# Performance work log

Measured on AMD Instinct MI355X. Metric: run time of the kernel, lower is better.

## Reference

```python
import jax, jax.numpy as jnp
import numpy as np

T_STEPS = 4096
N_CLASSES = 8192
TGT_LEN = 512
BLANK = 0
NEG = jnp.float32(-1e30)  # finite 'log zero' so grads stay nan-free


def setup_inputs() -> dict:
    key = jax.random.key(0)
    k1, k2 = jax.random.split(key)
    logits = jax.random.normal(k1, (T_STEPS, 1, N_CLASSES), dtype=jnp.float32)
    targets = jax.random.randint(k2, (TGT_LEN,), 0, N_CLASSES, dtype=jnp.int32)
    return {
        "logits": logits,
        "targets": targets,
        "input_lengths": T_STEPS,
        "target_lengths": TGT_LEN,
    }


def reference(logits, targets, input_lengths, target_lengths):
    # logits: [T, 1, C] -> log_probs [T, C]
    lp = jax.nn.log_softmax(logits, axis=2)[:, 0, :]
    L = target_lengths                      # static Python int
    tgt = targets[:L]
    S = 2 * L + 1
    # interleave blanks: [blank, y1, blank, y2, ..., blank]
    tw = jnp.full((S,), BLANK, dtype=tgt.dtype).at[1::2].set(tgt)

    # skip transition (s-2 -> s) allowed iff tw[s] != blank and tw[s] != tw[s-2]
    tw_m2 = jnp.concatenate([jnp.full((2,), -1, tw.dtype), tw[:-2]])
    allow_skip = (tw != BLANK) & (tw != tw_m2)

    # emission log-probs per state: [T, S]
    emit = lp[:, tw]

    alpha0 = jnp.full((S,), NEG).at[0].set(lp[0, BLANK])
    if S > 1:
        alpha0 = alpha0.at[1].set(lp[0, tw[1]])

    pad1 = jnp.full((1,), NEG)
    pad2 = jnp.full((2,), NEG)

    def step(a_prev, e_t):
        s1 = jnp.concatenate([pad1, a_prev[:-1]])
        s2 = jnp.concatenate([pad2, a_prev[:-2]])
        s2 = jnp.where(allow_skip, s2, NEG)
        a = jax.nn.logsumexp(jnp.stack([a_prev, s1, s2]), axis=0) + e_t
        return a, a

    _, alphas = jax.lax.scan(step, alpha0, emit[1:])
    alpha = jnp.concatenate([alpha0[None, :], alphas], axis=0)  # [T, S]

    final = jax.nn.logsumexp(alpha[input_lengths - 1, -2:])
    return -final
```

## Files before the change

### kernel.cpp

```cpp
#include <hip/hip_runtime.h>
#include <hip/hip_bf16.h>


#define T_STEPS 4096
#define N_CLASSES 8192
#define ROWB 2048
#define DG 12
#define DEPTH 16
#define INV_LN2 1.4426950408889634f
#define LN2F 0.6931471805599453f

static __device__ __forceinline__ float wredMax(float v) {
#pragma unroll
  for (int d = 32; d >= 1; d >>= 1) v = fmaxf(v, __shfl_xor(v, d, 64));
  return v;
}
static __device__ __forceinline__ float wredSum(float v) {
#pragma unroll
  for (int d = 32; d >= 1; d >>= 1) v += __shfl_xor(v, d, 64);
  return v;
}

#define FEXP2(x) __builtin_amdgcn_exp2f(x)
#define FLOG2(x) __builtin_amdgcn_logf(x)

__global__ __launch_bounds__(256) void ctc_emit(const float* __restrict__ logits,
                                                const int* __restrict__ targets,
                                                unsigned int* __restrict__ P,
                                                float* __restrict__ cvec) {
  __shared__ __align__(16) float row[N_CLASSES];
  __shared__ float red[4];
  const int t = blockIdx.x;
  const int tid = threadIdx.x;
  const int lane = tid & 63, wid = tid >> 6;
  const float4* src = (const float4*)(logits + (size_t)t * N_CLASSES);

  float4 v[8];
  float lmax = -3.0e38f;
#pragma unroll
  for (int k = 0; k < 8; ++k) {
    v[k] = src[tid + 256 * k];
    ((float4*)row)[tid + 256 * k] = v[k];
    lmax = fmaxf(lmax, fmaxf(fmaxf(v[k].x, v[k].y), fmaxf(v[k].z, v[k].w)));
  }
  lmax = wredMax(lmax);
  if (lane == 0) red[wid] = lmax;
  __syncthreads();
  const float rowmax = fmaxf(fmaxf(red[0], red[1]), fmaxf(red[2], red[3]));
  const float m2 = rowmax * INV_LN2;

  float acc = 0.f;
#pragma unroll
  for (int k = 0; k < 8; ++k) {
    acc += FEXP2(fmaf(v[k].x, INV_LN2, -m2));
    acc += FEXP2(fmaf(v[k].y, INV_LN2, -m2));
    acc += FEXP2(fmaf(v[k].z, INV_LN2, -m2));
    acc += FEXP2(fmaf(v[k].w, INV_LN2, -m2));
  }
  acc = wredSum(acc);
  __syncthreads();
  if (lane == 0) red[wid] = acc;
  __syncthreads();
  const float Z = red[0] + red[1] + red[2] + red[3];
  const float denom2 = m2 + FLOG2(Z);

  const float eb2 = fmaf(row[0], INV_LN2, -denom2);
  float et2[2];
  float gmax = eb2;
#pragma unroll
  for (int j = 0; j < 2; ++j) {
    const int p = tid + 256 * j;
    et2[j] = fmaf(row[targets[p]], INV_LN2, -denom2);
    gmax = fmaxf(gmax, et2[j]);
  }
  gmax = wredMax(gmax);
  __syncthreads();
  if (lane == 0) red[wid] = gmax;
  __syncthreads();
  const float ct = fmaxf(fmaxf(red[0], red[1]), fmaxf(red[2], red[3]));

  __hip_bfloat162* Prow = (__hip_bfloat162*)(P + (size_t)t * (ROWB / 4));
  __hip_bfloat162 pr;
  pr.x = __float2bfloat16(FEXP2(eb2 - ct));
#pragma unroll
  for (int j = 0; j < 2; ++j) {
    const int p = tid + 256 * j;
    pr.y = __float2bfloat16(FEXP2(et2[j] - ct));
    Prow[(p >> 3) | ((p & 7) << 6)] = pr;
  }
  if (tid == 0) cvec[t] = ct;
}

#define UNPK_LO(u) __uint_as_float((u) << 16)
#define UNPK_HI(u) __uint_as_float((u) & 0xFFFF0000u)

template <int DIRN>
static __device__ __forceinline__ void scan_half(const unsigned char* __restrict__ Pb,
                                                 const int* __restrict__ targets,
                                                 unsigned char* lbuf,
                                                 float* __restrict__ rawOut,
                                                 int* __restrict__ omOut) {
  const int lane = threadIdx.x;

  float al[8];
#pragma unroll
  for (int k = 0; k < 8; ++k) {
    const int kg = 8 * lane + k;
    if (DIRN == 0) {
      const int c = targets[kg];
      const int cm1 = (kg == 0) ? -1 : targets[kg - 1];
      al[k] = (c != 0 && c != cm1) ? 1.0f : 0.0f;
    } else {
      if (kg == 0) {
        al[k] = 0.0f;
      } else {
        const int c = targets[512 - kg];
        const int cm1 = targets[511 - kg];
        al[k] = (c != 0 && c != cm1) ? 1.0f : 0.0f;
      }
    }
  }

  float a[16], b[16], a16 = 0.f, b16;
#pragma unroll
  for (int j = 0; j < 16; ++j) a[j] = 0.f;
  if (lane == 0) {
    const unsigned int pv0 = *(const unsigned int*)(
        Pb + (DIRN ? ((size_t)(T_STEPS - 1) * ROWB + 4 * 511) : (size_t)0));
    a[0] = __uint_as_float((pv0 & 0xFFFFu) << 16);
    a[1] = __uint_as_float(pv0 & 0xFFFF0000u);
  }
  int omega = 0;
  int wprev = 0;
  int wd = 0;
  float Lraw = __shfl_up(a[15], 1, 64);

  const long long gstep = DIRN ? -(long long)ROWB : (long long)ROWB;
  const unsigned char* gp =
      Pb + (DIRN ? (size_t)(T_STEPS - 2) * ROWB : (size_t)ROWB) + 16 * lane;

#define STAGE_ROW(slot)                                                        \
  {                                                                            \
    unsigned char* lq = lbuf + (size_t)(slot) * ROWB;                          \
    __builtin_amdgcn_global_load_lds(                                          \
        (const __attribute__((address_space(1))) void*)gp,                     \
        (__attribute__((address_space(3))) void*)lq, 16, 0, 0);                \
    __builtin_amdgcn_global_load_lds(                                          \
        (const __attribute__((address_space(1))) void*)(gp + 1024),            \
        (__attribute__((address_space(3))) void*)(lq + 1024), 16, 0, 0);       \
    gp += gstep;                                                               \
  }

  const int rl = DIRN ? (63 - lane) : lane;

#define LOADSLOT(slot, R0, R1, R2, R3, R4, R5, R6, R7)                         \
  {                                                                            \
    const __attribute__((address_space(3))) unsigned int* sp =                 \
        (const __attribute__((address_space(3))) unsigned int*)(               \
            lbuf + (size_t)(slot) * ROWB);                                     \
    R0 = sp[rl + (DIRN ? 448 : 0)];                                            \
    R1 = sp[rl + (DIRN ? 384 : 64)];                                           \
    R2 = sp[rl + (DIRN ? 320 : 128)];                                          \
    R3 = sp[rl + (DIRN ? 256 : 192)];                                          \
    R4 = sp[rl + (DIRN ? 192 : 256)];                                          \
    R5 = sp[rl + (DIRN ? 128 : 320)];                                          \
    R6 = sp[rl + (DIRN ? 64 : 384)];                                           \
    R7 = sp[rl + (DIRN ? 0 : 448)];                                            \
  }

#pragma unroll
  for (int tt = 1; tt <= DG; ++tt) STAGE_ROW(tt & 15);

  unsigned int p0, p1, p2, p3, p4, p5, p6, p7;
  unsigned int q0, q1, q2, q3, q4, q5, q6, q7;
  asm volatile("s_waitcnt vmcnt(16)" ::: "memory");
  LOADSLOT(1, p0, p1, p2, p3, p4, p5, p6, p7);
  LOADSLOT(2, q0, q1, q2, q3, q4, q5, q6, q7);

  int t = 1;

#define STEP_HEAD(R0, R1, R2, R3, R4, R5, R6, R7)                              \
    const unsigned int x0 = R0, x1 = R1, x2 = R2, x3 = R3, x4 = R4, x5 = R5,   \
                       x6 = R6, x7 = R7;                                       \
    STAGE_ROW((t + DG) & 15);                                                  \
    asm volatile("s_waitcnt vmcnt(16)" ::: "memory");                          \
    LOADSLOT((t + 2) & 15, R0, R1, R2, R3, R4, R5, R6, R7);

#define BODY_MID(A, B)                                                         \
    B[2] = (A[2] + A[1]) * UNPK_LO(x1);                                        \
    B[3] = fmaf(al[1], A[1], A[3] + A[2]) * UNPK_HI(x1);                       \
    B[4] = (A[4] + A[3]) * UNPK_LO(x2);                                        \
    B[5] = fmaf(al[2], A[3], A[5] + A[4]) * UNPK_HI(x2);                       \
    B[6] = (A[6] + A[5]) * UNPK_LO(x3);                                        \
    B[7] = fmaf(al[3], A[5], A[7] + A[6]) * UNPK_HI(x3);                       \
    B[8] = (A[8] + A[7]) * UNPK_LO(x4);                                        \
    B[9] = fmaf(al[4], A[7], A[9] + A[8]) * UNPK_HI(x4);                       \
    B[10] = (A[10] + A[9]) * UNPK_LO(x5);                                      \
    B[11] = fmaf(al[5], A[9], A[11] + A[10]) * UNPK_HI(x5);                    \
    B[12] = (A[12] + A[11]) * UNPK_LO(x6);                                     \
    B[13] = fmaf(al[6], A[11], A[13] + A[12]) * UNPK_HI(x6);                   \
    B[14] = (A[14] + A[13]) * UNPK_LO(x7);

#define STEPF(A, A16, B, B16, R0, R1, R2, R3, R4, R5, R6, R7)                  \
  {                                                                            \
    STEP_HEAD(R0, R1, R2, R3, R4, R5, R6, R7)                                  \
    B[15] = fmaf(al[7], A[13], A[15] + A[14]) * UNPK_HI(x7);                   \
    B16 = (lane == 63) ? (A16 + A[15]) * UNPK_LO(x7) : 0.f;                    \
    float newL = __shfl_up(B[15], 1, 64);                                      \
    float La = (lane == 0) ? 0.f : ldexpf(Lraw, wd);                           \
    B[0] = (A[0] + La) * UNPK_LO(x0);                                          \
    B[1] = fmaf(al[0], La, A[1] + A[0]) * UNPK_HI(x0);                         \
    BODY_MID(A, B)                                                             \
    Lraw = newL;                                                               \
    ++t;                                                                       \
  }

#define STEPS(A, A16, B, B16, R0, R1, R2, R3, R4, R5, R6, R7)                  \
  {                                                                            \
    STEP_HEAD(R0, R1, R2, R3, R4, R5, R6, R7)                                  \
    float La = (lane == 0) ? 0.f : ldexpf(Lraw, wd);                           \
    B[15] = fmaf(al[7], A[13], A[15] + A[14]) * UNPK_HI(x7);                   \
    B16 = (lane == 63) ? (A16 + A[15]) * UNPK_LO(x7) : 0.f;                    \
    B[0] = (A[0] + La) * UNPK_LO(x0);                                          \
    B[1] = fmaf(al[0], La, A[1] + A[0]) * UNPK_HI(x0);                         \
    BODY_MID(A, B)                                                             \
    float m = 0.f;                                                             \
    _Pragma("unroll") for (int j = 0; j < 16; ++j) m = fmaxf(m, B[j]);         \
    if (lane == 63) m = fmaxf(m, B16);                                         \
    if (m > 0.f) {                                                             \
      const int e = (int)((__float_as_uint(m) >> 23) & 255u);                  \
      const int shift = 127 - e;                                               \
      _Pragma("unroll") for (int j = 0; j < 16; ++j) B[j] = ldexpf(B[j], shift); \
      B16 = ldexpf(B16, shift);                                                \
      omega += shift;                                                          \
    } else {                                                                   \
      omega = wprev;                                                           \
    }                                                                          \
    wprev = __shfl_up(omega, 1, 64);                                           \
    wd = omega - wprev;                                                        \
    Lraw = __shfl_up(B[15], 1, 64);                                            \
    ++t;                                                                       \
  }

  for (int g = 0; g < 255; ++g) {
    STEPF(a, a16, b, b16, p0, p1, p2, p3, p4, p5, p6, p7);
    STEPF(b, b16, a, a16, q0, q1, q2, q3, q4, q5, q6, q7);
    STEPF(a, a16, b, b16, p0, p1, p2, p3, p4, p5, p6, p7);
    STEPF(b, b16, a, a16, q0, q1, q2, q3, q4, q5, q6, q7);
    STEPF(a, a16, b, b16, p0, p1, p2, p3, p4, p5, p6, p7);
    STEPF(b, b16, a, a16, q0, q1, q2, q3, q4, q5, q6, q7);
    STEPF(a, a16, b, b16, p0, p1, p2, p3, p4, p5, p6, p7);
    STEPS(b, b16, a, a16, q0, q1, q2, q3, q4, q5, q6, q7);
  }
  STEPF(a, a16, b, b16, p0, p1, p2, p3, p4, p5, p6, p7);
  STEPF(b, b16, a, a16, q0, q1, q2, q3, q4, q5, q6, q7);
  STEPF(a, a16, b, b16, p0, p1, p2, p3, p4, p5, p6, p7);
  STEPF(b, b16, a, a16, q0, q1, q2, q3, q4, q5, q6, q7);
  STEPF(a, a16, b, b16, p0, p1, p2, p3, p4, p5, p6, p7);
  STEPF(b, b16, a, a16, q0, q1, q2, q3, q4, q5, q6, q7);
  STEPF(a, a16, b, b16, p0, p1, p2, p3, p4, p5, p6, p7);

#pragma unroll
  for (int j = 0; j < 16; ++j) rawOut[16 * lane + j] = b[j];
  if (lane == 63) rawOut[1024] = b16;
  omOut[lane] = omega;

#undef STEPS
#undef STEPF
#undef BODY_MID
#undef STEP_HEAD
#undef LOADSLOT
#undef STAGE_ROW
}

__global__ __launch_bounds__(64, 1) void ctc_scan2b(const unsigned char* __restrict__ Pb,
                                                    const int* __restrict__ targets,
                                                    float* __restrict__ rawF,
                                                    int* __restrict__ omF,
                                                    float* __restrict__ rawB,
                                                    int* __restrict__ omB) {
  __shared__ __align__(16) unsigned char lbuf[DEPTH * ROWB];
  if (blockIdx.x == 0)
    scan_half<0>(Pb, targets, lbuf, rawF, omF);
  else
    scan_half<1>(Pb, targets, lbuf, rawB, omB);
}

__global__ __launch_bounds__(64) void ctc_combine(const float* __restrict__ cvec,
                                                  const int* __restrict__ targets,
                                                  const float* __restrict__ rawF,
                                                  const int* __restrict__ omF,
                                                  const float* __restrict__ rawB,
                                                  const int* __restrict__ omB,
                                                  float* __restrict__ out) {
  __shared__ float vb[1025];
  const int lane = threadIdx.x;

  float sc = 0.f;
  for (int i = lane; i < T_STEPS; i += 64) sc += cvec[i];
  sc = wredSum(sc);

  const float wb = (float)omB[lane];
#pragma unroll
  for (int j = 0; j < 16; ++j) {
    const int st = 16 * lane + j;
    const float r = rawB[st];
    vb[1024 - st] = (r > 0.f) ? (FLOG2(r) - wb) : -1.0e30f;
  }
  if (lane == 63) {
    const float r = rawB[1024];
    vb[0] = (r > 0.f) ? (FLOG2(r) - wb) : -1.0e30f;
  }
  __syncthreads();

  const float wf = (float)omF[lane];
  float vloc[16];
  float m = -3.0e38f;
#pragma unroll
  for (int j = 0; j < 16; ++j) {
    const int s = 16 * lane + j;
    const float af = rawF[s];
    const float vf = (af > 0.f) ? (FLOG2(af) - wf) : -1.0e30f;
    const float g1 = vb[s];
    const float g2 = vb[s + 1];
    float g3 = -1.0e30f;
    if (s & 1) {
      const int k = (s - 1) >> 1;
      if (k + 1 < 512) {
        const int c = targets[k + 1];
        if (c != 0 && c != targets[k]) g3 = vb[s + 2];
      }
    }
    const float gm = fmaxf(g1, fmaxf(g2, g3));
    float gl = -1.0e30f;
    if (gm > -1.0e29f)
      gl = gm + FLOG2(FEXP2(g1 - gm) + FEXP2(g2 - gm) + FEXP2(g3 - gm));
    const float vv = vf + gl;
    vloc[j] = vv;
    m = fmaxf(m, vv);
  }
  float v16 = -3.0e38f;
  if (lane == 63) {
    const float af = rawF[1024];
    const float vf = (af > 0.f) ? (FLOG2(af) - wf) : -1.0e30f;
    v16 = vf + vb[1024];
    m = fmaxf(m, v16);
  }
  m = wredMax(m);
  float ssum = 0.f;
#pragma unroll
  for (int j = 0; j < 16; ++j) ssum += FEXP2(vloc[j] - m);
  if (lane == 63) ssum += FEXP2(v16 - m);
  ssum = wredSum(ssum);
  if (lane == 0) out[0] = -LN2F * (m + FLOG2(ssum) + sc);
}

extern "C" void kernel_launch(void* const* d_in, const int* in_sizes, int n_in,
                              void* d_out, int out_size, void* d_ws, size_t ws_size,
                              hipStream_t stream) {
  (void)in_sizes; (void)n_in; (void)out_size; (void)ws_size;
  const float* logits = (const float*)d_in[0];
  const int* targets = (const int*)d_in[1];
  char* ws = (char*)d_ws;
  unsigned int* P = (unsigned int*)ws;
  char* p = ws + (size_t)T_STEPS * ROWB;
  float* cvec = (float*)p;            p += T_STEPS * sizeof(float);
  float* rawF = (float*)p;            p += 1028 * sizeof(float);
  int* omF = (int*)p;                 p += 64 * sizeof(int);
  float* rawB = (float*)p;            p += 1028 * sizeof(float);
  int* omB = (int*)p;

  ctc_emit<<<dim3(T_STEPS), dim3(256), 0, stream>>>(logits, targets, P, cvec);
  ctc_scan2b<<<dim3(2), dim3(64), 0, stream>>>((const unsigned char*)P, targets,
                                               rawF, omF, rawB, omB);
  ctc_combine<<<dim3(1), dim3(64), 0, stream>>>(cvec, targets, rawF, omF, rawB, omB,
                                                (float*)d_out);
}
```

Before: 539.1 us.

## Vectorize LDS reads and deepen batched prefetch ring in CTC scan

Changes the emission row layout written by ctc_emit so that each lane's 8 packed bf16 pairs are contiguous, which lets the scan read them with two 128-bit LDS loads instead of eight 32-bit loads. The LDS staging ring grows from 16 to 32 rows, and prefetch is issued in batches of 8 rows once per 8-step group with a single waitcnt, replacing a per-step stage and wait. The aim is fewer LDS instructions and less wait overhead on the serial recurrence critical path. The cost is doubled LDS use (64KB) and a more complex ring-offset scheme where a prefetch or index mismatch would silently corrupt results.

```diff
diff --git a/kernel.cpp b/kernel.cpp
--- a/kernel.cpp
+++ b/kernel.cpp
@@ -5,10 +5,11 @@
 #define T_STEPS 4096
 #define N_CLASSES 8192
 #define ROWB 2048
-#define DG 12
-#define DEPTH 16
+#define RMASK 65535
 #define INV_LN2 1.4426950408889634f
 #define LN2F 0.6931471805599453f
+
+typedef unsigned int u32x4 __attribute__((ext_vector_type(4)));
 
 static __device__ __forceinline__ float wredMax(float v) {
 #pragma unroll
@@ -86,7 +87,7 @@
   for (int j = 0; j < 2; ++j) {
     const int p = tid + 256 * j;
     pr.y = __float2bfloat16(FEXP2(et2[j] - ct));
-    Prow[(p >> 3) | ((p & 7) << 6)] = pr;
+    Prow[((p & 4) << 6) | ((p >> 3) << 2) | (p & 3)] = pr;
   }
   if (tid == 0) cvec[t] = ct;
 }
@@ -139,9 +140,9 @@
   const unsigned char* gp =
       Pb + (DIRN ? (size_t)(T_STEPS - 2) * ROWB : (size_t)ROWB) + 16 * lane;
 
-#define STAGE_ROW(slot)                                                        \
+#define STAGE_ROW(ldsByte)                                                     \
   {                                                                            \
-    unsigned char* lq = lbuf + (size_t)(slot) * ROWB;                          \
+    unsigned char* lq = lbuf + (ldsByte);                                      \
     __builtin_amdgcn_global_load_lds(                                          \
         (const __attribute__((address_space(1))) void*)gp,                     \
         (__attribute__((address_space(3))) void*)lq, 16, 0, 0);                \
@@ -151,40 +152,34 @@
     gp += gstep;                                                               \
   }
 
-  const int rl = DIRN ? (63 - lane) : lane;
-
-#define LOADSLOT(slot, R0, R1, R2, R3, R4, R5, R6, R7)                         \
+  const int o1 = DIRN ? (1024 + 16 * (63 - lane)) : (16 * lane);
+  const int o2 = DIRN ? (16 * (63 - lane)) : (1024 + 16 * lane);
+
+#define LOADSLOT(ldsByte, RA, RB)                                              \
   {                                                                            \
-    const __attribute__((address_space(3))) unsigned int* sp =                 \
-        (const __attribute__((address_space(3))) unsigned int*)(               \
-            lbuf + (size_t)(slot) * ROWB);                                     \
-    R0 = sp[rl + (DIRN ? 448 : 0)];                                            \
-    R1 = sp[rl + (DIRN ? 384 : 64)];                                           \
-    R2 = sp[rl + (DIRN ? 320 : 128)];                                          \
-    R3 = sp[rl + (DIRN ? 256 : 192)];                                          \
-    R4 = sp[rl + (DIRN ? 192 : 256)];                                          \
-    R5 = sp[rl + (DIRN ? 128 : 320)];                                          \
-    R6 = sp[rl + (DIRN ? 64 : 384)];                                           \
-    R7 = sp[rl + (DIRN ? 0 : 448)];                                            \
-  }
-
-#pragma unroll
-  for (int tt = 1; tt <= DG; ++tt) STAGE_ROW(tt & 15);
-
-  unsigned int p0, p1, p2, p3, p4, p5, p6, p7;
-  unsigned int q0, q1, q2, q3, q4, q5, q6, q7;
-  asm volatile("s_waitcnt vmcnt(16)" ::: "memory");
-  LOADSLOT(1, p0, p1, p2, p3, p4, p5, p6, p7);
-  LOADSLOT(2, q0, q1, q2, q3, q4, q5, q6, q7);
-
-  int t = 1;
-
-#define STEP_HEAD(R0, R1, R2, R3, R4, R5, R6, R7)                              \
-    const unsigned int x0 = R0, x1 = R1, x2 = R2, x3 = R3, x4 = R4, x5 = R5,   \
-                       x6 = R6, x7 = R7;                                       \
-    STAGE_ROW((t + DG) & 15);                                                  \
-    asm volatile("s_waitcnt vmcnt(16)" ::: "memory");                          \
-    LOADSLOT((t + 2) & 15, R0, R1, R2, R3, R4, R5, R6, R7);
+    RA = *(const __attribute__((address_space(3))) u32x4*)(lbuf + (ldsByte) + o1); \
+    RB = *(const __attribute__((address_space(3))) u32x4*)(lbuf + (ldsByte) + o2); \
+  }
+
+  STAGE_ROW(0 * 2048)
+  STAGE_ROW(1 * 2048)
+#pragma unroll
+  for (int r = 3; r <= 26; ++r) STAGE_ROW((r - 1) * 2048)
+  asm volatile("s_waitcnt vmcnt(48)" ::: "memory");
+  u32x4 pA, pB, qA, qB;
+  LOADSLOT(0 * 2048, pA, pB)
+  LOADSLOT(1 * 2048, qA, qB)
+
+#define STEP_HEAD(RA, RB, LDSB)                                                \
+    unsigned int x0, x1, x2, x3, x4, x5, x6, x7;                               \
+    if (DIRN == 0) {                                                           \
+      x0 = RA.x; x1 = RA.y; x2 = RA.z; x3 = RA.w;                              \
+      x4 = RB.x; x5 = RB.y; x6 = RB.z; x7 = RB.w;                              \
+    } else {                                                                   \
+      x0 = RA.w; x1 = RA.z; x2 = RA.y; x3 = RA.x;                              \
+      x4 = RB.w; x5 = RB.z; x6 = RB.y; x7 = RB.x;                              \
+    }                                                                          \
+    LOADSLOT(LDSB, RA, RB)
 
 #define BODY_MID(A, B)                                                         \
     B[2] = (A[2] + A[1]) * UNPK_LO(x1);                                        \
@@ -201,9 +196,9 @@
     B[13] = fmaf(al[6], A[11], A[13] + A[12]) * UNPK_HI(x6);                   \
     B[14] = (A[14] + A[13]) * UNPK_LO(x7);
 
-#define STEPF(A, A16, B, B16, R0, R1, R2, R3, R4, R5, R6, R7)                  \
+#define STEPF(A, A16, B, B16, RA, RB, LDSB)                                    \
   {                                                                            \
-    STEP_HEAD(R0, R1, R2, R3, R4, R5, R6, R7)                                  \
+    STEP_HEAD(RA, RB, LDSB)                                                    \
     B[15] = fmaf(al[7], A[13], A[15] + A[14]) * UNPK_HI(x7);                   \
     B16 = (lane == 63) ? (A16 + A[15]) * UNPK_LO(x7) : 0.f;                    \
     float newL = __shfl_up(B[15], 1, 64);                                      \
@@ -212,12 +207,11 @@
     B[1] = fmaf(al[0], La, A[1] + A[0]) * UNPK_HI(x0);                         \
     BODY_MID(A, B)                                                             \
     Lraw = newL;                                                               \
-    ++t;                                                                       \
-  }
-
-#define STEPS(A, A16, B, B16, R0, R1, R2, R3, R4, R5, R6, R7)                  \
+  }
+
+#define STEPS(A, A16, B, B16, RA, RB, LDSB)                                    \
   {                                                                            \
-    STEP_HEAD(R0, R1, R2, R3, R4, R5, R6, R7)                                  \
+    STEP_HEAD(RA, RB, LDSB)                                                    \
     float La = (lane == 0) ? 0.f : ldexpf(Lraw, wd);                           \
     B[15] = fmaf(al[7], A[13], A[15] + A[14]) * UNPK_HI(x7);                   \
     B16 = (lane == 63) ? (A16 + A[15]) * UNPK_LO(x7) : 0.f;                    \
@@ -239,26 +233,37 @@
     wprev = __shfl_up(omega, 1, 64);                                           \
     wd = omega - wprev;                                                        \
     Lraw = __shfl_up(B[15], 1, 64);                                            \
-    ++t;                                                                       \
-  }
-
+  }
+
+  int sbase = 0;
   for (int g = 0; g < 255; ++g) {
-    STEPF(a, a16, b, b16, p0, p1, p2, p3, p4, p5, p6, p7);
-    STEPF(b, b16, a, a16, q0, q1, q2, q3, q4, q5, q6, q7);
-    STEPF(a, a16, b, b16, p0, p1, p2, p3, p4, p5, p6, p7);
-    STEPF(b, b16, a, a16, q0, q1, q2, q3, q4, q5, q6, q7);
-    STEPF(a, a16, b, b16, p0, p1, p2, p3, p4, p5, p6, p7);
-    STEPF(b, b16, a, a16, q0, q1, q2, q3, q4, q5, q6, q7);
-    STEPF(a, a16, b, b16, p0, p1, p2, p3, p4, p5, p6, p7);
-    STEPS(b, b16, a, a16, q0, q1, q2, q3, q4, q5, q6, q7);
-  }
-  STEPF(a, a16, b, b16, p0, p1, p2, p3, p4, p5, p6, p7);
-  STEPF(b, b16, a, a16, q0, q1, q2, q3, q4, q5, q6, q7);
-  STEPF(a, a16, b, b16, p0, p1, p2, p3, p4, p5, p6, p7);
-  STEPF(b, b16, a, a16, q0, q1, q2, q3, q4, q5, q6, q7);
-  STEPF(a, a16, b, b16, p0, p1, p2, p3, p4, p5, p6, p7);
-  STEPF(b, b16, a, a16, q0, q1, q2, q3, q4, q5, q6, q7);
-  STEPF(a, a16, b, b16, p0, p1, p2, p3, p4, p5, p6, p7);
+    asm volatile("s_waitcnt vmcnt(32)" ::: "memory");
+    STAGE_ROW((sbase + 26 * 2048) & RMASK)
+    STAGE_ROW((sbase + 27 * 2048) & RMASK)
+    STAGE_ROW((sbase + 28 * 2048) & RMASK)
+    STAGE_ROW((sbase + 29 * 2048) & RMASK)
+    STAGE_ROW((sbase + 30 * 2048) & RMASK)
+    STAGE_ROW((sbase + 31 * 2048) & RMASK)
+    STAGE_ROW((sbase + 32 * 2048) & RMASK)
+    STAGE_ROW((sbase + 33 * 2048) & RMASK)
+    STEPF(a, a16, b, b16, pA, pB, (sbase + 2 * 2048) & RMASK);
+    STEPF(b, b16, a, a16, qA, qB, (sbase + 3 * 2048) & RMASK);
+    STEPF(a, a16, b, b16, pA, pB, (sbase + 4 * 2048) & RMASK);
+    STEPF(b, b16, a, a16, qA, qB, (sbase + 5 * 2048) & RMASK);
+    STEPF(a, a16, b, b16, pA, pB, (sbase + 6 * 2048) & RMASK);
+    STEPF(b, b16, a, a16, qA, qB, (sbase + 7 * 2048) & RMASK);
+    STEPF(a, a16, b, b16, pA, pB, (sbase + 8 * 2048) & RMASK);
+    STEPS(b, b16, a, a16, qA, qB, (sbase + 9 * 2048) & RMASK);
+    sbase = (sbase + 16384) & RMASK;
+  }
+  asm volatile("s_waitcnt vmcnt(32)" ::: "memory");
+  STEPF(a, a16, b, b16, pA, pB, (sbase + 2 * 2048) & RMASK);
+  STEPF(b, b16, a, a16, qA, qB, (sbase + 3 * 2048) & RMASK);
+  STEPF(a, a16, b, b16, pA, pB, (sbase + 4 * 2048) & RMASK);
+  STEPF(b, b16, a, a16, qA, qB, (sbase + 5 * 2048) & RMASK);
+  STEPF(a, a16, b, b16, pA, pB, (sbase + 6 * 2048) & RMASK);
+  STEPF(b, b16, a, a16, qA, qB, (sbase + 7 * 2048) & RMASK);
+  STEPF(a, a16, b, b16, pA, pB, (sbase + 8 * 2048) & RMASK);
 
 #pragma unroll
   for (int j = 0; j < 16; ++j) rawOut[16 * lane + j] = b[j];
@@ -279,7 +284,7 @@
                                                     int* __restrict__ omF,
                                                     float* __restrict__ rawB,
                                                     int* __restrict__ omB) {
-  __shared__ __align__(16) unsigned char lbuf[DEPTH * ROWB];
+  __shared__ __align__(16) unsigned char lbuf[32 * ROWB];
   if (blockIdx.x == 0)
     scan_half<0>(Pb, targets, lbuf, rawF, omF);
   else
```

Result: faster. 524.2 us (-2.8%).

## Split each CTC scan direction across two waves with LDS handoff and barriers

Applied to the files above, without the earlier changes.

Each direction's alpha/beta scan now runs on 128 threads (two wavefronts), and each thread holds 8 states instead of 16. The boundary value and its scale exponent pass from wave 0 to wave 1 through LDS, with a workgroup barrier on every time step. The emission table is also compacted: the blank probability, which is the same for every state in a row, goes into a separate per-timestep array, so each row of P shrinks from 2048 to 1024 bytes and the stride-permuted layout is removed. The aim is to halve the serial arithmetic per step, at the cost of one barrier per step and a deeper 64-row LDS prefetch ring.

```diff
diff --git a/kernel.cpp b/kernel.cpp
--- a/kernel.cpp
+++ b/kernel.cpp
@@ -4,12 +4,12 @@
 
 #define T_STEPS 4096
 #define N_CLASSES 8192
-#define ROWB 2048
-#define DG 12
-#define DEPTH 16
+#define ROWB 1024
 #define INV_LN2 1.4426950408889634f
 #define LN2F 0.6931471805599453f
 
+typedef unsigned int u32x2 __attribute__((ext_vector_type(2)));
+
 static __device__ __forceinline__ float wredMax(float v) {
 #pragma unroll
   for (int d = 32; d >= 1; d >>= 1) v = fmaxf(v, __shfl_xor(v, d, 64));
@@ -23,10 +23,13 @@
 
 #define FEXP2(x) __builtin_amdgcn_exp2f(x)
 #define FLOG2(x) __builtin_amdgcn_logf(x)
+#define UNPK_LO(u) __uint_as_float((u) << 16)
+#define UNPK_HI(u) __uint_as_float((u) & 0xFFFF0000u)
 
 __global__ __launch_bounds__(256) void ctc_emit(const float* __restrict__ logits,
                                                 const int* __restrict__ targets,
                                                 unsigned int* __restrict__ P,
+                                                float* __restrict__ pbArr,
                                                 float* __restrict__ cvec) {
   __shared__ __align__(16) float row[N_CLASSES];
   __shared__ float red[4];
@@ -65,225 +68,222 @@
   const float denom2 = m2 + FLOG2(Z);
 
   const float eb2 = fmaf(row[0], INV_LN2, -denom2);
-  float et2[2];
-  float gmax = eb2;
-#pragma unroll
-  for (int j = 0; j < 2; ++j) {
-    const int p = tid + 256 * j;
-    et2[j] = fmaf(row[targets[p]], INV_LN2, -denom2);
-    gmax = fmaxf(gmax, et2[j]);
-  }
+  const float e0 = fmaf(row[targets[2 * tid]], INV_LN2, -denom2);
+  const float e1 = fmaf(row[targets[2 * tid + 1]], INV_LN2, -denom2);
+  float gmax = fmaxf(eb2, fmaxf(e0, e1));
   gmax = wredMax(gmax);
   __syncthreads();
   if (lane == 0) red[wid] = gmax;
   __syncthreads();
   const float ct = fmaxf(fmaxf(red[0], red[1]), fmaxf(red[2], red[3]));
 
-  __hip_bfloat162* Prow = (__hip_bfloat162*)(P + (size_t)t * (ROWB / 4));
   __hip_bfloat162 pr;
-  pr.x = __float2bfloat16(FEXP2(eb2 - ct));
-#pragma unroll
-  for (int j = 0; j < 2; ++j) {
-    const int p = tid + 256 * j;
-    pr.y = __float2bfloat16(FEXP2(et2[j] - ct));
-    Prow[(p >> 3) | ((p & 7) << 6)] = pr;
-  }
-  if (tid == 0) cvec[t] = ct;
-}
-
-#define UNPK_LO(u) __uint_as_float((u) << 16)
-#define UNPK_HI(u) __uint_as_float((u) & 0xFFFF0000u)
+  pr.x = __float2bfloat16(FEXP2(e0 - ct));
+  pr.y = __float2bfloat16(FEXP2(e1 - ct));
+  ((__hip_bfloat162*)(P + (size_t)t * (ROWB / 4)))[tid] = pr;
+  if (tid == 0) {
+    cvec[t] = ct;
+    pbArr[t] = FEXP2(eb2 - ct);
+  }
+}
+
+#define PBB 65536
+#define RLB 66048
 
 template <int DIRN>
 static __device__ __forceinline__ void scan_half(const unsigned char* __restrict__ Pb,
+                                                 const float* __restrict__ pbArr,
                                                  const int* __restrict__ targets,
                                                  unsigned char* lbuf,
                                                  float* __restrict__ rawOut,
                                                  int* __restrict__ omOut) {
-  const int lane = threadIdx.x;
-
-  float al[8];
-#pragma unroll
-  for (int k = 0; k < 8; ++k) {
-    const int kg = 8 * lane + k;
+  const int tid = threadIdx.x;
+  const int lane = tid & 63;
+  const int w = tid >> 6;
+  const bool isTop = (tid == 127);
+  const int rowoff = DIRN ? (1016 - 8 * tid) : (8 * tid);
+
+  float al[4];
+#pragma unroll
+  for (int k = 0; k < 4; ++k) {
+    const int kg = 4 * tid + k;
     if (DIRN == 0) {
       const int c = targets[kg];
       const int cm1 = (kg == 0) ? -1 : targets[kg - 1];
       al[k] = (c != 0 && c != cm1) ? 1.0f : 0.0f;
     } else {
-      if (kg == 0) {
-        al[k] = 0.0f;
-      } else {
+      if (kg == 0) al[k] = 0.0f;
+      else {
         const int c = targets[512 - kg];
-        const int cm1 = targets[511 - kg];
-        al[k] = (c != 0 && c != cm1) ? 1.0f : 0.0f;
+        al[k] = (c != 0 && c != targets[511 - kg]) ? 1.0f : 0.0f;
       }
     }
   }
 
-  float a[16], b[16], a16 = 0.f, b16;
-#pragma unroll
-  for (int j = 0; j < 16; ++j) a[j] = 0.f;
-  if (lane == 0) {
-    const unsigned int pv0 = *(const unsigned int*)(
-        Pb + (DIRN ? ((size_t)(T_STEPS - 1) * ROWB + 4 * 511) : (size_t)0));
-    a[0] = __uint_as_float((pv0 & 0xFFFFu) << 16);
-    a[1] = __uint_as_float(pv0 & 0xFFFF0000u);
-  }
-  int omega = 0;
-  int wprev = 0;
-  int wd = 0;
-  float Lraw = __shfl_up(a[15], 1, 64);
-
-  const long long gstep = DIRN ? -(long long)ROWB : (long long)ROWB;
-  const unsigned char* gp =
-      Pb + (DIRN ? (size_t)(T_STEPS - 2) * ROWB : (size_t)ROWB) + 16 * lane;
-
-#define STAGE_ROW(slot)                                                        \
-  {                                                                            \
-    unsigned char* lq = lbuf + (size_t)(slot) * ROWB;                          \
+  float a[8], b[8], a16 = 0.f, b16;
+#pragma unroll
+  for (int j = 0; j < 8; ++j) a[j] = 0.f;
+  if (tid == 0) {
+    if (DIRN == 0) {
+      const unsigned int d0 = *(const unsigned int*)(Pb);
+      a[0] = pbArr[0];
+      a[1] = UNPK_LO(d0);
+    } else {
+      const unsigned int d = *(const unsigned int*)(Pb + (size_t)4095 * ROWB + 4 * 255);
+      a[0] = pbArr[4095];
+      a[1] = UNPK_HI(d);
+    }
+  }
+  int omega = 0, wprev = 0, wd = 0;
+  float Lraw = __shfl_up(a[7], 1, 64);
+
+#define STAGE_STEP(rr)                                                         \
+  { const int r_ = (rr);                                                       \
+    const unsigned char* gs_ = Pb + ((size_t)(DIRN ? (4095 - r_) : r_) << 10) + 16 * lane; \
     __builtin_amdgcn_global_load_lds(                                          \
-        (const __attribute__((address_space(1))) void*)gp,                     \
-        (__attribute__((address_space(3))) void*)lq, 16, 0, 0);                \
+        (const __attribute__((address_space(1))) void*)gs_,                    \
+        (__attribute__((address_space(3))) void*)(lbuf + ((r_ & 63) << 10)),   \
+        16, 0, 0); }
+
+#define STAGE_PB(cc)                                                           \
+  { const int c_ = (cc);                                                       \
+    const float* ps_ = pbArr + (DIRN ? (4094 - 64 * c_ - lane) : (64 * c_ + 1 + lane)); \
     __builtin_amdgcn_global_load_lds(                                          \
-        (const __attribute__((address_space(1))) void*)(gp + 1024),            \
-        (__attribute__((address_space(3))) void*)(lq + 1024), 16, 0, 0);       \
-    gp += gstep;                                                               \
-  }
-
-  const int rl = DIRN ? (63 - lane) : lane;
-
-#define LOADSLOT(slot, R0, R1, R2, R3, R4, R5, R6, R7)                         \
-  {                                                                            \
-    const __attribute__((address_space(3))) unsigned int* sp =                 \
-        (const __attribute__((address_space(3))) unsigned int*)(               \
-            lbuf + (size_t)(slot) * ROWB);                                     \
-    R0 = sp[rl + (DIRN ? 448 : 0)];                                            \
-    R1 = sp[rl + (DIRN ? 384 : 64)];                                           \
-    R2 = sp[rl + (DIRN ? 320 : 128)];                                          \
-    R3 = sp[rl + (DIRN ? 256 : 192)];                                          \
-    R4 = sp[rl + (DIRN ? 192 : 256)];                                          \
-    R5 = sp[rl + (DIRN ? 128 : 320)];                                          \
-    R6 = sp[rl + (DIRN ? 64 : 384)];                                           \
-    R7 = sp[rl + (DIRN ? 0 : 448)];                                            \
-  }
-
-#pragma unroll
-  for (int tt = 1; tt <= DG; ++tt) STAGE_ROW(tt & 15);
-
-  unsigned int p0, p1, p2, p3, p4, p5, p6, p7;
-  unsigned int q0, q1, q2, q3, q4, q5, q6, q7;
-  asm volatile("s_waitcnt vmcnt(16)" ::: "memory");
-  LOADSLOT(1, p0, p1, p2, p3, p4, p5, p6, p7);
-  LOADSLOT(2, q0, q1, q2, q3, q4, q5, q6, q7);
-
-  int t = 1;
-
-#define STEP_HEAD(R0, R1, R2, R3, R4, R5, R6, R7)                              \
-    const unsigned int x0 = R0, x1 = R1, x2 = R2, x3 = R3, x4 = R4, x5 = R5,   \
-                       x6 = R6, x7 = R7;                                       \
-    STAGE_ROW((t + DG) & 15);                                                  \
-    asm volatile("s_waitcnt vmcnt(16)" ::: "memory");                          \
-    LOADSLOT((t + 2) & 15, R0, R1, R2, R3, R4, R5, R6, R7);
-
-#define BODY_MID(A, B)                                                         \
-    B[2] = (A[2] + A[1]) * UNPK_LO(x1);                                        \
-    B[3] = fmaf(al[1], A[1], A[3] + A[2]) * UNPK_HI(x1);                       \
-    B[4] = (A[4] + A[3]) * UNPK_LO(x2);                                        \
-    B[5] = fmaf(al[2], A[3], A[5] + A[4]) * UNPK_HI(x2);                       \
-    B[6] = (A[6] + A[5]) * UNPK_LO(x3);                                        \
-    B[7] = fmaf(al[3], A[5], A[7] + A[6]) * UNPK_HI(x3);                       \
-    B[8] = (A[8] + A[7]) * UNPK_LO(x4);                                        \
-    B[9] = fmaf(al[4], A[7], A[9] + A[8]) * UNPK_HI(x4);                       \
-    B[10] = (A[10] + A[9]) * UNPK_LO(x5);                                      \
-    B[11] = fmaf(al[5], A[9], A[11] + A[10]) * UNPK_HI(x5);                    \
-    B[12] = (A[12] + A[11]) * UNPK_LO(x6);                                     \
-    B[13] = fmaf(al[6], A[11], A[13] + A[12]) * UNPK_HI(x6);                   \
-    B[14] = (A[14] + A[13]) * UNPK_LO(x7);
-
-#define STEPF(A, A16, B, B16, R0, R1, R2, R3, R4, R5, R6, R7)                  \
-  {                                                                            \
-    STEP_HEAD(R0, R1, R2, R3, R4, R5, R6, R7)                                  \
-    B[15] = fmaf(al[7], A[13], A[15] + A[14]) * UNPK_HI(x7);                   \
-    B16 = (lane == 63) ? (A16 + A[15]) * UNPK_LO(x7) : 0.f;                    \
-    float newL = __shfl_up(B[15], 1, 64);                                      \
-    float La = (lane == 0) ? 0.f : ldexpf(Lraw, wd);                           \
-    B[0] = (A[0] + La) * UNPK_LO(x0);                                          \
-    B[1] = fmaf(al[0], La, A[1] + A[0]) * UNPK_HI(x0);                         \
-    BODY_MID(A, B)                                                             \
+        (const __attribute__((address_space(1))) void*)ps_,                    \
+        (__attribute__((address_space(3))) void*)(lbuf + PBB + ((c_ & 1) << 8)), \
+        4, 0, 0); }
+
+#pragma unroll
+  for (int k = 0; k < 4; ++k) {
+    const int rb = 8 * k + 1 + 4 * w;
+    STAGE_STEP(rb) STAGE_STEP(rb + 1) STAGE_STEP(rb + 2) STAGE_STEP(rb + 3)
+  }
+  if (w == 0) STAGE_PB(0)
+  asm volatile("s_waitcnt vmcnt(0)" ::: "memory");
+  if (tid >= 64 && tid < 68) {
+    u32x2 z; z.x = 0u; z.y = 0u;
+    *(__attribute__((address_space(3))) u32x2*)(lbuf + RLB + ((tid - 64) << 3)) = z;
+  }
+  asm volatile("s_waitcnt lgkmcnt(0)" ::: "memory");
+  __builtin_amdgcn_s_barrier();
+  asm volatile("" ::: "memory");
+
+  u32x2 dP = *(const __attribute__((address_space(3))) u32x2*)(lbuf + 1024 + rowoff);
+  u32x2 dQ = *(const __attribute__((address_space(3))) u32x2*)(lbuf + 2048 + rowoff);
+  float pbP = *(const __attribute__((address_space(3))) float*)(lbuf + PBB + 0);
+  float pbQ = *(const __attribute__((address_space(3))) float*)(lbuf + PBB + 4);
+
+#define ENDBAR                                                                 \
+    asm volatile("s_waitcnt lgkmcnt(0)" ::: "memory");                         \
+    __builtin_amdgcn_s_barrier();                                              \
+    asm volatile("" ::: "memory");
+
+#define STEP_TOP(A, A16, B, B16, D01, PBR, JJ)                                 \
+    const unsigned int x0 = D01.x, x1 = D01.y;                                 \
+    const float pbc = PBR;                                                     \
+    D01 = *(const __attribute__((address_space(3))) u32x2*)(                   \
+        lbuf + ((sb + ((JJ) + 2) * 1024) & 65535) + rowoff);                   \
+    PBR = *(const __attribute__((address_space(3))) float*)(                   \
+        lbuf + PBB + (((t0 + (JJ) + 1) & 127) << 2));                          \
+    const u32x2 pay = *(const __attribute__((address_space(3))) u32x2*)(       \
+        lbuf + RLB + ((((JJ)-1) & 3) << 3));                                   \
+    const float H3 = DIRN ? UNPK_LO(x0) : UNPK_HI(x1);                         \
+    B[7] = fmaf(al[3], A[5], A[7] + A[6]) * H3;                                \
+    if (tid == 63) {                                                           \
+      u32x2 wv; wv.x = __float_as_uint(B[7]); wv.y = (unsigned)omega;          \
+      *(__attribute__((address_space(3))) u32x2*)(lbuf + RLB + (((JJ)&3) << 3)) = wv; \
+    }                                                                          \
+    float newL = __shfl_up(B[7], 1, 64);                                       \
+    const float H0 = DIRN ? UNPK_HI(x1) : UNPK_LO(x0);                         \
+    const float H1 = DIRN ? UNPK_LO(x1) : UNPK_HI(x0);                         \
+    const float H2 = DIRN ? UNPK_HI(x0) : UNPK_LO(x1);                         \
+    B[4] = (A[4] + A[3]) * pbc;                                                \
+    B[5] = fmaf(al[2], A[3], A[5] + A[4]) * H2;                                \
+    B[6] = (A[6] + A[5]) * pbc;                                                \
+    B16 = isTop ? (A16 + A[7]) * pbc : 0.f;                                    \
+    const float Lsc = ldexpf(Lraw, wd);                                        \
+    const float Lre = ldexpf(__uint_as_float(pay.x), omega - (int)pay.y);      \
+    const float La = (lane != 0) ? Lsc : ((tid == 0) ? 0.f : Lre);             \
+    B[0] = (A[0] + La) * pbc;                                                  \
+    B[1] = fmaf(al[0], La, A[1] + A[0]) * H0;                                  \
+    B[2] = (A[2] + A[1]) * pbc;                                                \
+    B[3] = fmaf(al[1], A[1], A[3] + A[2]) * H1;
+
+#define STEPF(A, A16, B, B16, D01, PBR, JJ)                                    \
+  { STEP_TOP(A, A16, B, B16, D01, PBR, JJ)                                     \
     Lraw = newL;                                                               \
-    ++t;                                                                       \
-  }
-
-#define STEPS(A, A16, B, B16, R0, R1, R2, R3, R4, R5, R6, R7)                  \
-  {                                                                            \
-    STEP_HEAD(R0, R1, R2, R3, R4, R5, R6, R7)                                  \
-    float La = (lane == 0) ? 0.f : ldexpf(Lraw, wd);                           \
-    B[15] = fmaf(al[7], A[13], A[15] + A[14]) * UNPK_HI(x7);                   \
-    B16 = (lane == 63) ? (A16 + A[15]) * UNPK_LO(x7) : 0.f;                    \
-    B[0] = (A[0] + La) * UNPK_LO(x0);                                          \
-    B[1] = fmaf(al[0], La, A[1] + A[0]) * UNPK_HI(x0);                         \
-    BODY_MID(A, B)                                                             \
+    ENDBAR }
+
+#define STEPS(A, A16, B, B16, D01, PBR, JJ)                                    \
+  { STEP_TOP(A, A16, B, B16, D01, PBR, JJ)                                     \
+    (void)newL;                                                                \
+    if (tid == 64) wprev = (int)pay.y;    \
     float m = 0.f;                                                             \
-    _Pragma("unroll") for (int j = 0; j < 16; ++j) m = fmaxf(m, B[j]);         \
-    if (lane == 63) m = fmaxf(m, B16);                                         \
+    _Pragma("unroll") for (int j = 0; j < 8; ++j) m = fmaxf(m, B[j]);          \
+    if (isTop) m = fmaxf(m, B16);                                              \
     if (m > 0.f) {                                                             \
       const int e = (int)((__float_as_uint(m) >> 23) & 255u);                  \
-      const int shift = 127 - e;                                               \
-      _Pragma("unroll") for (int j = 0; j < 16; ++j) B[j] = ldexpf(B[j], shift); \
-      B16 = ldexpf(B16, shift);                                                \
-      omega += shift;                                                          \
-    } else {                                                                   \
-      omega = wprev;                                                           \
-    }                                                                          \
+      const int sh = 127 - e;                                                  \
+      _Pragma("unroll") for (int j = 0; j < 8; ++j) B[j] = ldexpf(B[j], sh);   \
+      B16 = ldexpf(B16, sh);                                                   \
+      omega += sh;                                                             \
+    } else omega = wprev;                                                      \
     wprev = __shfl_up(omega, 1, 64);                                           \
     wd = omega - wprev;                                                        \
-    Lraw = __shfl_up(B[15], 1, 64);                                            \
-    ++t;                                                                       \
-  }
-
-  for (int g = 0; g < 255; ++g) {
-    STEPF(a, a16, b, b16, p0, p1, p2, p3, p4, p5, p6, p7);
-    STEPF(b, b16, a, a16, q0, q1, q2, q3, q4, q5, q6, q7);
-    STEPF(a, a16, b, b16, p0, p1, p2, p3, p4, p5, p6, p7);
-    STEPF(b, b16, a, a16, q0, q1, q2, q3, q4, q5, q6, q7);
-    STEPF(a, a16, b, b16, p0, p1, p2, p3, p4, p5, p6, p7);
-    STEPF(b, b16, a, a16, q0, q1, q2, q3, q4, q5, q6, q7);
-    STEPF(a, a16, b, b16, p0, p1, p2, p3, p4, p5, p6, p7);
-    STEPS(b, b16, a, a16, q0, q1, q2, q3, q4, q5, q6, q7);
-  }
-  STEPF(a, a16, b, b16, p0, p1, p2, p3, p4, p5, p6, p7);
-  STEPF(b, b16, a, a16, q0, q1, q2, q3, q4, q5, q6, q7);
-  STEPF(a, a16, b, b16, p0, p1, p2, p3, p4, p5, p6, p7);
-  STEPF(b, b16, a, a16, q0, q1, q2, q3, q4, q5, q6, q7);
-  STEPF(a, a16, b, b16, p0, p1, p2, p3, p4, p5, p6, p7);
-  STEPF(b, b16, a, a16, q0, q1, q2, q3, q4, q5, q6, q7);
-  STEPF(a, a16, b, b16, p0, p1, p2, p3, p4, p5, p6, p7);
-
-#pragma unroll
-  for (int j = 0; j < 16; ++j) rawOut[16 * lane + j] = b[j];
-  if (lane == 63) rawOut[1024] = b16;
-  omOut[lane] = omega;
+    Lraw = __shfl_up(B[7], 1, 64);                                             \
+    ENDBAR }
+
+  int t0 = 0, sb = 0;
+  for (int G = 0; G < 255; ++G) {
+    asm volatile("s_waitcnt vmcnt(4)" ::: "memory");
+    { const int rb = t0 + 33 + 4 * w;
+      STAGE_STEP(rb) STAGE_STEP(rb + 1) STAGE_STEP(rb + 2) STAGE_STEP(rb + 3) }
+    if (w == 0 && (G & 7) == 0) STAGE_PB((G >> 3) + 1)
+    STEPF(a, a16, b, b16, dP, pbP, 1)
+    STEPF(b, b16, a, a16, dQ, pbQ, 2)
+    STEPF(a, a16, b, b16, dP, pbP, 3)
+    STEPF(b, b16, a, a16, dQ, pbQ, 4)
+    STEPF(a, a16, b, b16, dP, pbP, 5)
+    STEPF(b, b16, a, a16, dQ, pbQ, 6)
+    STEPF(a, a16, b, b16, dP, pbP, 7)
+    STEPS(b, b16, a, a16, dQ, pbQ, 8)
+    t0 += 8;
+    sb = (sb + 8192) & 65535;
+  }
+  asm volatile("s_waitcnt vmcnt(4)" ::: "memory");
+  STEPF(a, a16, b, b16, dP, pbP, 1)
+  STEPF(b, b16, a, a16, dQ, pbQ, 2)
+  STEPF(a, a16, b, b16, dP, pbP, 3)
+  STEPF(b, b16, a, a16, dQ, pbQ, 4)
+  STEPF(a, a16, b, b16, dP, pbP, 5)
+  STEPF(b, b16, a, a16, dQ, pbQ, 6)
+  STEPF(a, a16, b, b16, dP, pbP, 7)
+
+#pragma unroll
+  for (int j = 0; j < 8; ++j) rawOut[8 * tid + j] = b[j];
+  if (tid == 127) rawOut[1024] = b16;
+  omOut[tid] = omega;
 
 #undef STEPS
 #undef STEPF
-#undef BODY_MID
-#undef STEP_HEAD
-#undef LOADSLOT
-#undef STAGE_ROW
-}
-
-__global__ __launch_bounds__(64, 1) void ctc_scan2b(const unsigned char* __restrict__ Pb,
-                                                    const int* __restrict__ targets,
-                                                    float* __restrict__ rawF,
-                                                    int* __restrict__ omF,
-                                                    float* __restrict__ rawB,
-                                                    int* __restrict__ omB) {
-  __shared__ __align__(16) unsigned char lbuf[DEPTH * ROWB];
+#undef STEP_TOP
+#undef ENDBAR
+#undef STAGE_PB
+#undef STAGE_STEP
+}
+
+__global__ __launch_bounds__(128, 1) void ctc_scan2w(const unsigned char* __restrict__ Pb,
+                                                     const float* __restrict__ pbArr,
+                                                     const int* __restrict__ targets,
+                                                     float* __restrict__ rawF,
+                                                     int* __restrict__ omF,
+                                                     float* __restrict__ rawB,
+                                                     int* __restrict__ omB) {
+  __shared__ __align__(16) unsigned char lbuf[66112];
   if (blockIdx.x == 0)
-    scan_half<0>(Pb, targets, lbuf, rawF, omF);
+    scan_half<0>(Pb, pbArr, targets, lbuf, rawF, omF);
   else
-    scan_half<1>(Pb, targets, lbuf, rawB, omB);
+    scan_half<1>(Pb, pbArr, targets, lbuf, rawB, omB);
 }
 
 __global__ __launch_bounds__(64) void ctc_combine(const float* __restrict__ cvec,
@@ -300,26 +300,30 @@
   for (int i = lane; i < T_STEPS; i += 64) sc += cvec[i];
   sc = wredSum(sc);
 
-  const float wb = (float)omB[lane];
+  const float wb0 = (float)omB[2 * lane];
+  const float wb1 = (float)omB[2 * lane + 1];
 #pragma unroll
   for (int j = 0; j < 16; ++j) {
     const int st = 16 * lane + j;
     const float r = rawB[st];
+    const float wb = (j < 8) ? wb0 : wb1;
     vb[1024 - st] = (r > 0.f) ? (FLOG2(r) - wb) : -1.0e30f;
   }
   if (lane == 63) {
     const float r = rawB[1024];
-    vb[0] = (r > 0.f) ? (FLOG2(r) - wb) : -1.0e30f;
-  }
-  __syncthreads();
-
-  const float wf = (float)omF[lane];
+    vb[0] = (r > 0.f) ? (FLOG2(r) - (float)omB[127]) : -1.0e30f;
+  }
+  __syncthreads();
+
+  const float wf0 = (float)omF[2 * lane];
+  const float wf1 = (float)omF[2 * lane + 1];
   float vloc[16];
   float m = -3.0e38f;
 #pragma unroll
   for (int j = 0; j < 16; ++j) {
     const int s = 16 * lane + j;
     const float af = rawF[s];
+    const float wf = (j < 8) ? wf0 : wf1;
     const float vf = (af > 0.f) ? (FLOG2(af) - wf) : -1.0e30f;
     const float g1 = vb[s];
     const float g2 = vb[s + 1];
@@ -342,7 +346,7 @@
   float v16 = -3.0e38f;
   if (lane == 63) {
     const float af = rawF[1024];
-    const float vf = (af > 0.f) ? (FLOG2(af) - wf) : -1.0e30f;
+    const float vf = (af > 0.f) ? (FLOG2(af) - (float)omF[127]) : -1.0e30f;
     v16 = vf + vb[1024];
     m = fmaxf(m, v16);
   }
@@ -363,16 +367,16 @@
   const int* targets = (const int*)d_in[1];
   char* ws = (char*)d_ws;
   unsigned int* P = (unsigned int*)ws;
-  char* p = ws + (size_t)T_STEPS * ROWB;
-  float* cvec = (float*)p;            p += T_STEPS * sizeof(float);
-  float* rawF = (float*)p;            p += 1028 * sizeof(float);
-  int* omF = (int*)p;                 p += 64 * sizeof(int);
-  float* rawB = (float*)p;            p += 1028 * sizeof(float);
-  int* omB = (int*)p;
-
-  ctc_emit<<<dim3(T_STEPS), dim3(256), 0, stream>>>(logits, targets, P, cvec);
-  ctc_scan2b<<<dim3(2), dim3(64), 0, stream>>>((const unsigned char*)P, targets,
-                                               rawF, omF, rawB, omB);
+  float* pbArr = (float*)(ws + (size_t)T_STEPS * ROWB);
+  float* cvec = pbArr + T_STEPS;
+  float* rawF = cvec + T_STEPS;
+  int* omF = (int*)(rawF + 1028);
+  float* rawB = (float*)(omF + 128);
+  int* omB = (int*)(rawB + 1028);
+
+  ctc_emit<<<dim3(T_STEPS), dim3(256), 0, stream>>>(logits, targets, P, pbArr, cvec);
+  ctc_scan2w<<<dim3(2), dim3(128), 0, stream>>>((const unsigned char*)P, pbArr,
+                                                targets, rawF, omF, rawB, omB);
   ctc_combine<<<dim3(1), dim3(64), 0, stream>>>(cvec, targets, rawF, omF, rawB, omB,
                                                 (float*)d_out);
 }
```

Result: faster. 518.2 us (-3.9%).
